# Kernel tuning notes

Measured on AMD Instinct MI355X. Metric: run time of the kernel, lower is better.

Reference implementation:

```python
import jax, jax.numpy as jnp
import numpy as np

N_AGENT = 25
N_S = 32
N_A = 4
HID = 128
EHH_HID = HID * N_AGENT          # 3200
INTER = 150                      # INTERMEDIATE_NODES
BATCH = 2048
N_EDGE = 300


def _leaky(x):
    return jnp.where(x >= 0, x, 0.01 * x)


def setup_inputs() -> dict:
    key = jax.random.key(0)
    ks = jax.random.split(key, 12)
    states = jax.random.normal(ks[0], (N_AGENT, BATCH, N_S), dtype=jnp.float32)
    ehh_w = jax.random.normal(ks[1], (N_AGENT * N_S, EHH_HID), dtype=jnp.float32) * 0.05
    anova = jax.random.normal(ks[2], (EHH_HID + INTER, N_AGENT), dtype=jnp.float32)
    w1 = jax.random.normal(ks[3], (N_AGENT, EHH_HID, 12), dtype=jnp.float32) * 0.02
    b1 = jax.random.normal(ks[4], (N_AGENT, 12), dtype=jnp.float32) * 0.02
    w2 = jax.random.normal(ks[5], (N_AGENT, 12, 12), dtype=jnp.float32) * 0.3
    b2 = jax.random.normal(ks[6], (N_AGENT, 12), dtype=jnp.float32) * 0.02
    w3 = jax.random.normal(ks[7], (N_AGENT, 12, N_A), dtype=jnp.float32) * 0.3
    b3 = jax.random.normal(ks[8], (N_AGENT, N_A), dtype=jnp.float32) * 0.02
    actions = jax.random.randint(ks[9], (N_AGENT, BATCH), 0, N_A, dtype=jnp.int32)
    # adjacency rows: (bi_att_row, neighbor_row_a, unused, neighbor_row_b)
    c0 = jax.random.randint(ks[10], (N_EDGE, 1), 0, INTER, dtype=jnp.int32)
    c13 = jax.random.randint(ks[11], (N_EDGE, 2), 0, EHH_HID, dtype=jnp.int32)
    adj = jnp.concatenate([c0, c13[:, :1], jnp.zeros((N_EDGE, 1), jnp.int32), c13[:, 1:]], axis=1)
    return {"states": states, "ehh_w": ehh_w, "anova": anova,
            "w1": w1, "b1": b1, "w2": w2, "b2": b2, "w3": w3, "b3": b3,
            "actions": actions, "adj": adj}


def reference(states, ehh_w, anova, w1, b1, w2, b2, w3, b3, actions, adj):
    # states: (A, B, S) -> ehh_s: (B, A*S)   (torch.cat(states, dim=1))
    B = states.shape[1]
    ehh_s = jnp.transpose(states, (1, 0, 2)).reshape(B, -1)
    # EHH normalization (BatchNorm, affine=False, batch stats) + linear + LeakyReLU
    mu = jnp.mean(ehh_s, axis=0, keepdims=True)
    var = jnp.var(ehh_s, axis=0, keepdims=True)
    ehh_n = (ehh_s - mu) * jax.lax.rsqrt(var + 1e-5)
    ehh_embedding = _leaky(ehh_n @ ehh_w)                    # (B, EHH_HID)

    # ANOVA attention assembly via adjacency scatter
    self_att = anova[:EHH_HID, :]                            # (EHH_HID, A)
    bi_att = anova[EHH_HID:, :]                              # (INTER, A)
    vals = bi_att[adj[:, 0], :]                              # (E, A)
    neighbor_att = jnp.zeros((EHH_HID, N_AGENT), jnp.float32)
    neighbor_att = neighbor_att.at[adj[:, 1]].set(vals)
    neighbor_att = neighbor_att.at[adj[:, 3]].set(vals)
    all_att = (self_att + neighbor_att).T                    # (A, EHH_HID)

    # att_s repeat/permute/reshape == broadcast of embedding per agent
    att_out = ehh_embedding[:, None, :] * all_att[None, :, :]  # (B, A, EHH_HID)

    # per-agent critics (ehh_hidden -> 12 -> 12 -> n_a)
    h1 = _leaky(jnp.einsum('bah,ahk->bak', att_out, w1) + b1[None])
    h2 = _leaky(jnp.einsum('bak,akj->baj', h1, w2) + b2[None])
    all_q = jnp.einsum('baj,ajc->bac', h2, w3) + b3[None]     # (B, A, N_A)

    # q = all_q.gather(1, in_acs) per agent -> (A, B)
    q = jnp.take_along_axis(all_q, actions.T[:, :, None], axis=2)[..., 0].T
    return q
```

## Files before the change

### kernel.cpp

```cpp
#include <hip/hip_runtime.h>
#include <cstdint>

#define NAG 25
#define NS 32
#define EHH 3200
#define KDIM 800
#define BATCH 2048
#define NEDGE 300
#define NPAD 384
#define KSPLIT 5

typedef _Float16 half8 __attribute__((ext_vector_type(8)));
typedef float f32x4 __attribute__((ext_vector_type(4)));

__device__ __forceinline__ float leaky(float x) { return x >= 0.f ? x : 0.01f * x; }

__global__ void init_kernel(float* __restrict__ acc, int* __restrict__ winner) {
    int t = blockIdx.x * 256 + threadIdx.x;
    if (t < 1600) acc[t] = 0.f;
    if (t < EHH) winner[t] = -1;
}

__global__ void stats_part(const float* __restrict__ states, float* __restrict__ acc) {
    int a = blockIdx.x;
    int chunk = blockIdx.y;
    int s = threadIdx.x & 31, ty = threadIdx.x >> 5;
    const float* base = states + ((size_t)a * BATCH + chunk * 128) * NS + s;
    float sum = 0.f, sq = 0.f;
    for (int b = ty; b < 128; b += 8) {
        float v = base[(size_t)b * NS];
        sum += v; sq += v * v;
    }
    __shared__ float ls[8][32], lq[8][32];
    ls[ty][s] = sum; lq[ty][s] = sq;
    __syncthreads();
    if (ty == 0) {
#pragma unroll
        for (int i = 1; i < 8; ++i) { sum += ls[i][s]; sq += lq[i][s]; }
        atomicAdd(&acc[a * 32 + s], sum);
        atomicAdd(&acc[800 + a * 32 + s], sq);
    }
}

__global__ void prep_kernel(const float* __restrict__ states, const float* __restrict__ acc,
                            const float* __restrict__ ehh_w, const int* __restrict__ adj,
                            int* __restrict__ winner,
                            _Float16* __restrict__ A, _Float16* __restrict__ wt) {
    __shared__ float tile[32][33];
    int bi = blockIdx.x;
    if (bi < 6400) {
        int t = bi * 256 + threadIdx.x;
        int b = t / KDIM;
        int f = t - b * KDIM;
        int a = f >> 5, s = f & 31;
        float m = acc[f] * (1.f / BATCH);
        float var = acc[800 + f] * (1.f / BATCH) - m * m;
        float rs = rsqrtf(var + 1e-5f);
        float v = states[((size_t)a * BATCH + b) * NS + s];
        A[t] = (_Float16)((v - m) * rs);
    } else if (bi < 8900) {
        int bb = bi - 6400;
        int n0 = (bb % 100) * 32, k0 = (bb / 100) * 32;
        int x = threadIdx.x & 31, y = threadIdx.x >> 5;
        for (int i = y; i < 32; i += 8)
            tile[i][x] = ehh_w[(size_t)(k0 + i) * EHH + n0 + x];
        __syncthreads();
        for (int i = y; i < 32; i += 8)
            wt[(size_t)(n0 + i) * KDIM + k0 + x] = (_Float16)tile[x][i];
    } else {
        int e = (bi - 8900) * 256 + threadIdx.x;
        if (e < 2 * NEDGE) {
            int pass = e >= NEDGE;
            int ee = pass ? e - NEDGE : e;
            int dest = adj[ee * 4 + (pass ? 3 : 1)];
            atomicMax(&winner[dest], e);
        }
    }
}

__global__ void w2d_kernel(const float* __restrict__ anova, const int* __restrict__ adj,
                           const int* __restrict__ winner, const float* __restrict__ w1,
                           _Float16* __restrict__ w2dt) {
    if (blockIdx.x < 313) {
        int t = blockIdx.x * 256 + threadIdx.x;
        if (t < NAG * EHH) {
            int a = t / EHH;
            int h = t - a * EHH;
            float att = anova[(size_t)h * NAG + a];
            int w = winner[h];
            if (w >= 0) {
                int ee = w >= NEDGE ? w - NEDGE : w;
                att += anova[(size_t)(EHH + adj[ee * 4]) * NAG + a];
            }
            const float* wp = w1 + ((size_t)a * EHH + h) * 12;
#pragma unroll
            for (int kk = 0; kk < 12; ++kk)
                w2dt[(size_t)(a * 12 + kk) * EHH + h] = (_Float16)(att * wp[kk]);
        }
    } else {
        int p = (blockIdx.x - 313) * 256 + threadIdx.x;
        if (p < (NPAD - 300) * EHH / 8) {
            half8 z = {0, 0, 0, 0, 0, 0, 0, 0};
            ((half8*)(w2dt + (size_t)300 * EHH))[p] = z;
        }
    }
}

__device__ __forceinline__ void async16(const void* g, void* l) {
    __builtin_amdgcn_global_load_lds(
        (const __attribute__((address_space(1))) void*)(uintptr_t)g,
        (__attribute__((address_space(3))) void*)(unsigned)(uintptr_t)l, 16, 0, 0);
}

template <bool LEAKY_F16_OUT>
__global__ __launch_bounds__(256)
void gemm_bt(const _Float16* __restrict__ A, const _Float16* __restrict__ B,
             _Float16* __restrict__ Ch, float* __restrict__ Cf,
             int Ktot, int ldc, int kPerSplit, int slabStride) {
    __shared__ __attribute__((aligned(16))) _Float16 As[2][128 * 32];
    __shared__ __attribute__((aligned(16))) _Float16 Bs[2][128 * 32];
    const int tid = threadIdx.x;
    const int lane = tid & 63;
    const int wave = tid >> 6;
    const int wm = (wave >> 1) << 6;
    const int wn = (wave & 1) << 6;
    const int m0 = blockIdx.x << 7;
    const int n0 = blockIdx.y << 7;
    const int k0 = blockIdx.z * kPerSplit;
    const int nk = kPerSplit >> 5;

    const int srow = lane >> 2;
    const int scol = (lane & 3) << 3;
    const _Float16* gA0 = A + (size_t)(m0 + wave * 16 + srow) * Ktot + k0 + scol;
    const _Float16* gA1 = gA0 + (size_t)64 * Ktot;
    const _Float16* gB0 = B + (size_t)(n0 + wave * 16 + srow) * Ktot + k0 + scol;
    const _Float16* gB1 = gB0 + (size_t)64 * Ktot;
    const int lofs = wave * 512;

    f32x4 acc[4][4];
    const f32x4 zero = {0.f, 0.f, 0.f, 0.f};
#pragma unroll
    for (int i = 0; i < 4; ++i)
#pragma unroll
        for (int j = 0; j < 4; ++j) acc[i][j] = zero;

    const int fr = lane & 15;
    const int q8 = (lane >> 4) << 3;

    async16(gA0, As[0] + lofs);
    async16(gA1, As[0] + 2048 + lofs);
    async16(gB0, Bs[0] + lofs);
    async16(gB1, Bs[0] + 2048 + lofs);

    for (int kt = 0; kt < nk; ++kt) {
        const int cur = kt & 1;
        __syncthreads();
        if (kt + 1 < nk) {
            const int ko = (kt + 1) << 5;
            const int nxt = cur ^ 1;
            async16(gA0 + ko, As[nxt] + lofs);
            async16(gA1 + ko, As[nxt] + 2048 + lofs);
            async16(gB0 + ko, Bs[nxt] + lofs);
            async16(gB1 + ko, Bs[nxt] + 2048 + lofs);
        }
        half8 av[4], bv[4];
#pragma unroll
        for (int i = 0; i < 4; ++i)
            av[i] = *(const half8*)(As[cur] + (wm + i * 16 + fr) * 32 + q8);
#pragma unroll
        for (int j = 0; j < 4; ++j)
            bv[j] = *(const half8*)(Bs[cur] + (wn + j * 16 + fr) * 32 + q8);
#pragma unroll
        for (int i = 0; i < 4; ++i)
#pragma unroll
            for (int j = 0; j < 4; ++j)
                acc[i][j] = __builtin_amdgcn_mfma_f32_16x16x32_f16(av[i], bv[j], acc[i][j], 0, 0, 0);
    }

    const int r0 = (lane >> 4) << 2;
    if (LEAKY_F16_OUT) {
#pragma unroll
        for (int i = 0; i < 4; ++i)
#pragma unroll
            for (int j = 0; j < 4; ++j)
#pragma unroll
                for (int r = 0; r < 4; ++r) {
                    int row = m0 + wm + i * 16 + r0 + r;
                    int col = n0 + wn + j * 16 + fr;
                    Ch[(size_t)row * ldc + col] = (_Float16)leaky(acc[i][j][r]);
                }
    } else {
        float* C = Cf + (size_t)blockIdx.z * slabStride;
#pragma unroll
        for (int i = 0; i < 4; ++i)
#pragma unroll
            for (int j = 0; j < 4; ++j)
#pragma unroll
                for (int r = 0; r < 4; ++r) {
                    int row = m0 + wm + i * 16 + r0 + r;
                    int col = n0 + wn + j * 16 + fr;
                    C[(size_t)row * ldc + col] = acc[i][j][r];
                }
    }
}

__global__ void tail_kernel(const float* __restrict__ Hp, const float* __restrict__ b1,
                            const float* __restrict__ w2, const float* __restrict__ b2,
                            const float* __restrict__ w3, const float* __restrict__ b3,
                            const int* __restrict__ act, float* __restrict__ out) {
    int t = blockIdx.x * 256 + threadIdx.x;
    int b = t & (BATCH - 1);
    int a = t >> 11;
    const float* hp = Hp + (size_t)b * NPAD + a * 12;
    float h1[12];
#pragma unroll
    for (int k = 0; k < 12; ++k) {
        float s = b1[a * 12 + k];
#pragma unroll
        for (int ks = 0; ks < KSPLIT; ++ks) s += hp[(size_t)ks * BATCH * NPAD + k];
        h1[k] = leaky(s);
    }
    float h2[12];
#pragma unroll
    for (int j = 0; j < 12; ++j) {
        float s = b2[a * 12 + j];
#pragma unroll
        for (int k = 0; k < 12; ++k) s += h1[k] * w2[(a * 12 + k) * 12 + j];
        h2[j] = leaky(s);
    }
    int c = act[t];
    float q = b3[a * 4 + c];
#pragma unroll
    for (int j = 0; j < 12; ++j) q += h2[j] * w3[(a * 12 + j) * 4 + c];
    out[t] = q;
}

extern "C" void kernel_launch(void* const* d_in, const int* in_sizes, int n_in,
                              void* d_out, int out_size, void* d_ws, size_t ws_size,
                              hipStream_t stream) {
    (void)in_sizes; (void)n_in; (void)out_size; (void)ws_size;
    const float* states = (const float*)d_in[0];
    const float* ehh_w  = (const float*)d_in[1];
    const float* anova  = (const float*)d_in[2];
    const float* w1     = (const float*)d_in[3];
    const float* b1     = (const float*)d_in[4];
    const float* w2     = (const float*)d_in[5];
    const float* b2     = (const float*)d_in[6];
    const float* w3     = (const float*)d_in[7];
    const float* b3     = (const float*)d_in[8];
    const int* actions  = (const int*)d_in[9];
    const int* adj      = (const int*)d_in[10];
    float* out = (float*)d_out;

    char* ws = (char*)d_ws;
    float*     acc    = (float*)    (ws + 0);
    int*       winner = (int*)      (ws + 8192);
    _Float16*  Abf    = (_Float16*) (ws + 32768);
    _Float16*  WbT    = (_Float16*) (ws + 3311616);
    _Float16*  W2dT   = (_Float16*) (ws + 8433664);
    _Float16*  emb    = (_Float16*) (ws + 10893312);
    float*     Hp     = (float*)    (ws + 24002560);

    init_kernel<<<13, 256, 0, stream>>>(acc, winner);
    stats_part<<<dim3(25, 16), 256, 0, stream>>>(states, acc);
    prep_kernel<<<8903, 256, 0, stream>>>(states, acc, ehh_w, adj, winner, Abf, WbT);
    w2d_kernel<<<445, 256, 0, stream>>>(anova, adj, winner, w1, W2dT);
    gemm_bt<true><<<dim3(16, 25, 1), 256, 0, stream>>>(Abf, WbT, emb, nullptr, KDIM, EHH, KDIM, 0);
    gemm_bt<false><<<dim3(16, 3, KSPLIT), 256, 0, stream>>>(emb, W2dT, nullptr, Hp, EHH, NPAD,
                                                            EHH / KSPLIT, BATCH * NPAD);
    tail_kernel<<<(BATCH * NAG) / 256, 256, 0, stream>>>(Hp, b1, w2, b2, w3, b3, actions, out);
}
```

Before: 143.9 us.

## Fuse all stages into one persistent kernel with software grid barriers

Replaces seven kernel launches with one persistent 256-block kernel plus a counter-init kernel, separating stages with atomic-counter grid barriers. Stats accumulation now writes per-chunk partials instead of using atomics, and the adjacency winner scan becomes a serial per-column loop. This removes launch overhead and inter-kernel gaps. In exchange the grid is limited to 256 blocks, so the large prep and GEMM stages run in a grid-stride loop with less parallelism, barrier spinning adds cost, and correctness depends on all 256 blocks being co-resident.

```diff
diff --git a/kernel.cpp b/kernel.cpp
--- a/kernel.cpp
+++ b/kernel.cpp
@@ -2,109 +2,18 @@
 #include <cstdint>
 
 #define NAG 25
-#define NS 32
 #define EHH 3200
 #define KDIM 800
 #define BATCH 2048
 #define NEDGE 300
 #define NPAD 384
 #define KSPLIT 5
+#define GRID 256
 
 typedef _Float16 half8 __attribute__((ext_vector_type(8)));
 typedef float f32x4 __attribute__((ext_vector_type(4)));
 
 __device__ __forceinline__ float leaky(float x) { return x >= 0.f ? x : 0.01f * x; }
-
-__global__ void init_kernel(float* __restrict__ acc, int* __restrict__ winner) {
-    int t = blockIdx.x * 256 + threadIdx.x;
-    if (t < 1600) acc[t] = 0.f;
-    if (t < EHH) winner[t] = -1;
-}
-
-__global__ void stats_part(const float* __restrict__ states, float* __restrict__ acc) {
-    int a = blockIdx.x;
-    int chunk = blockIdx.y;
-    int s = threadIdx.x & 31, ty = threadIdx.x >> 5;
-    const float* base = states + ((size_t)a * BATCH + chunk * 128) * NS + s;
-    float sum = 0.f, sq = 0.f;
-    for (int b = ty; b < 128; b += 8) {
-        float v = base[(size_t)b * NS];
-        sum += v; sq += v * v;
-    }
-    __shared__ float ls[8][32], lq[8][32];
-    ls[ty][s] = sum; lq[ty][s] = sq;
-    __syncthreads();
-    if (ty == 0) {
-#pragma unroll
-        for (int i = 1; i < 8; ++i) { sum += ls[i][s]; sq += lq[i][s]; }
-        atomicAdd(&acc[a * 32 + s], sum);
-        atomicAdd(&acc[800 + a * 32 + s], sq);
-    }
-}
-
-__global__ void prep_kernel(const float* __restrict__ states, const float* __restrict__ acc,
-                            const float* __restrict__ ehh_w, const int* __restrict__ adj,
-                            int* __restrict__ winner,
-                            _Float16* __restrict__ A, _Float16* __restrict__ wt) {
-    __shared__ float tile[32][33];
-    int bi = blockIdx.x;
-    if (bi < 6400) {
-        int t = bi * 256 + threadIdx.x;
-        int b = t / KDIM;
-        int f = t - b * KDIM;
-        int a = f >> 5, s = f & 31;
-        float m = acc[f] * (1.f / BATCH);
-        float var = acc[800 + f] * (1.f / BATCH) - m * m;
-        float rs = rsqrtf(var + 1e-5f);
-        float v = states[((size_t)a * BATCH + b) * NS + s];
-        A[t] = (_Float16)((v - m) * rs);
-    } else if (bi < 8900) {
-        int bb = bi - 6400;
-        int n0 = (bb % 100) * 32, k0 = (bb / 100) * 32;
-        int x = threadIdx.x & 31, y = threadIdx.x >> 5;
-        for (int i = y; i < 32; i += 8)
-            tile[i][x] = ehh_w[(size_t)(k0 + i) * EHH + n0 + x];
-        __syncthreads();
-        for (int i = y; i < 32; i += 8)
-            wt[(size_t)(n0 + i) * KDIM + k0 + x] = (_Float16)tile[x][i];
-    } else {
-        int e = (bi - 8900) * 256 + threadIdx.x;
-        if (e < 2 * NEDGE) {
-            int pass = e >= NEDGE;
-            int ee = pass ? e - NEDGE : e;
-            int dest = adj[ee * 4 + (pass ? 3 : 1)];
-            atomicMax(&winner[dest], e);
-        }
-    }
-}
-
-__global__ void w2d_kernel(const float* __restrict__ anova, const int* __restrict__ adj,
-                           const int* __restrict__ winner, const float* __restrict__ w1,
-                           _Float16* __restrict__ w2dt) {
-    if (blockIdx.x < 313) {
-        int t = blockIdx.x * 256 + threadIdx.x;
-        if (t < NAG * EHH) {
-            int a = t / EHH;
-            int h = t - a * EHH;
-            float att = anova[(size_t)h * NAG + a];
-            int w = winner[h];
-            if (w >= 0) {
-                int ee = w >= NEDGE ? w - NEDGE : w;
-                att += anova[(size_t)(EHH + adj[ee * 4]) * NAG + a];
-            }
-            const float* wp = w1 + ((size_t)a * EHH + h) * 12;
-#pragma unroll
-            for (int kk = 0; kk < 12; ++kk)
-                w2dt[(size_t)(a * 12 + kk) * EHH + h] = (_Float16)(att * wp[kk]);
-        }
-    } else {
-        int p = (blockIdx.x - 313) * 256 + threadIdx.x;
-        if (p < (NPAD - 300) * EHH / 8) {
-            half8 z = {0, 0, 0, 0, 0, 0, 0, 0};
-            ((half8*)(w2dt + (size_t)300 * EHH))[p] = z;
-        }
-    }
-}
 
 __device__ __forceinline__ void async16(const void* g, void* l) {
     __builtin_amdgcn_global_load_lds(
@@ -112,23 +21,29 @@
         (__attribute__((address_space(3))) void*)(unsigned)(uintptr_t)l, 16, 0, 0);
 }
 
+__device__ __forceinline__ void gbar(int* c) {
+    __syncthreads();
+    __threadfence();
+    if (threadIdx.x == 0) {
+        atomicAdd(c, 1);
+        while (__hip_atomic_load(c, __ATOMIC_ACQUIRE, __HIP_MEMORY_SCOPE_AGENT) < GRID)
+            __builtin_amdgcn_s_sleep(8);
+    }
+    __syncthreads();
+    __threadfence();
+}
+
+__global__ void binit(int* cnt) { if (threadIdx.x < 8) cnt[threadIdx.x] = 0; }
+
 template <bool LEAKY_F16_OUT>
-__global__ __launch_bounds__(256)
-void gemm_bt(const _Float16* __restrict__ A, const _Float16* __restrict__ B,
-             _Float16* __restrict__ Ch, float* __restrict__ Cf,
-             int Ktot, int ldc, int kPerSplit, int slabStride) {
-    __shared__ __attribute__((aligned(16))) _Float16 As[2][128 * 32];
-    __shared__ __attribute__((aligned(16))) _Float16 Bs[2][128 * 32];
-    const int tid = threadIdx.x;
+__device__ void gemm_tile(const _Float16* __restrict__ A, const _Float16* __restrict__ B,
+                          _Float16* __restrict__ Ch, float* __restrict__ Cf,
+                          int Ktot, int ldc, int nk, int m0, int n0, int k0,
+                          _Float16* As, _Float16* Bs, int tid) {
     const int lane = tid & 63;
     const int wave = tid >> 6;
     const int wm = (wave >> 1) << 6;
     const int wn = (wave & 1) << 6;
-    const int m0 = blockIdx.x << 7;
-    const int n0 = blockIdx.y << 7;
-    const int k0 = blockIdx.z * kPerSplit;
-    const int nk = kPerSplit >> 5;
-
     const int srow = lane >> 2;
     const int scol = (lane & 3) << 3;
     const _Float16* gA0 = A + (size_t)(m0 + wave * 16 + srow) * Ktot + k0 + scol;
@@ -147,29 +62,30 @@
     const int fr = lane & 15;
     const int q8 = (lane >> 4) << 3;
 
-    async16(gA0, As[0] + lofs);
-    async16(gA1, As[0] + 2048 + lofs);
-    async16(gB0, Bs[0] + lofs);
-    async16(gB1, Bs[0] + 2048 + lofs);
+    __syncthreads();
+    async16(gA0, As + lofs);
+    async16(gA1, As + 2048 + lofs);
+    async16(gB0, Bs + lofs);
+    async16(gB1, Bs + 2048 + lofs);
 
     for (int kt = 0; kt < nk; ++kt) {
-        const int cur = kt & 1;
+        const int cur = (kt & 1) * 4096;
         __syncthreads();
         if (kt + 1 < nk) {
             const int ko = (kt + 1) << 5;
-            const int nxt = cur ^ 1;
-            async16(gA0 + ko, As[nxt] + lofs);
-            async16(gA1 + ko, As[nxt] + 2048 + lofs);
-            async16(gB0 + ko, Bs[nxt] + lofs);
-            async16(gB1 + ko, Bs[nxt] + 2048 + lofs);
+            const int nxt = 4096 - cur;
+            async16(gA0 + ko, As + nxt + lofs);
+            async16(gA1 + ko, As + nxt + 2048 + lofs);
+            async16(gB0 + ko, Bs + nxt + lofs);
+            async16(gB1 + ko, Bs + nxt + 2048 + lofs);
         }
         half8 av[4], bv[4];
 #pragma unroll
         for (int i = 0; i < 4; ++i)
-            av[i] = *(const half8*)(As[cur] + (wm + i * 16 + fr) * 32 + q8);
+            av[i] = *(const half8*)(As + cur + (wm + i * 16 + fr) * 32 + q8);
 #pragma unroll
         for (int j = 0; j < 4; ++j)
-            bv[j] = *(const half8*)(Bs[cur] + (wn + j * 16 + fr) * 32 + q8);
+            bv[j] = *(const half8*)(Bs + cur + (wn + j * 16 + fr) * 32 + q8);
 #pragma unroll
         for (int i = 0; i < 4; ++i)
 #pragma unroll
@@ -178,61 +94,174 @@
     }
 
     const int r0 = (lane >> 4) << 2;
-    if (LEAKY_F16_OUT) {
-#pragma unroll
-        for (int i = 0; i < 4; ++i)
-#pragma unroll
-            for (int j = 0; j < 4; ++j)
-#pragma unroll
-                for (int r = 0; r < 4; ++r) {
-                    int row = m0 + wm + i * 16 + r0 + r;
-                    int col = n0 + wn + j * 16 + fr;
+#pragma unroll
+    for (int i = 0; i < 4; ++i)
+#pragma unroll
+        for (int j = 0; j < 4; ++j)
+#pragma unroll
+            for (int r = 0; r < 4; ++r) {
+                int row = m0 + wm + i * 16 + r0 + r;
+                int col = n0 + wn + j * 16 + fr;
+                if (LEAKY_F16_OUT)
                     Ch[(size_t)row * ldc + col] = (_Float16)leaky(acc[i][j][r]);
-                }
-    } else {
-        float* C = Cf + (size_t)blockIdx.z * slabStride;
-#pragma unroll
-        for (int i = 0; i < 4; ++i)
-#pragma unroll
-            for (int j = 0; j < 4; ++j)
-#pragma unroll
-                for (int r = 0; r < 4; ++r) {
-                    int row = m0 + wm + i * 16 + r0 + r;
-                    int col = n0 + wn + j * 16 + fr;
-                    C[(size_t)row * ldc + col] = acc[i][j][r];
-                }
-    }
-}
-
-__global__ void tail_kernel(const float* __restrict__ Hp, const float* __restrict__ b1,
-                            const float* __restrict__ w2, const float* __restrict__ b2,
-                            const float* __restrict__ w3, const float* __restrict__ b3,
-                            const int* __restrict__ act, float* __restrict__ out) {
-    int t = blockIdx.x * 256 + threadIdx.x;
-    int b = t & (BATCH - 1);
-    int a = t >> 11;
-    const float* hp = Hp + (size_t)b * NPAD + a * 12;
-    float h1[12];
-#pragma unroll
-    for (int k = 0; k < 12; ++k) {
-        float s = b1[a * 12 + k];
-#pragma unroll
-        for (int ks = 0; ks < KSPLIT; ++ks) s += hp[(size_t)ks * BATCH * NPAD + k];
-        h1[k] = leaky(s);
-    }
-    float h2[12];
-#pragma unroll
-    for (int j = 0; j < 12; ++j) {
-        float s = b2[a * 12 + j];
-#pragma unroll
-        for (int k = 0; k < 12; ++k) s += h1[k] * w2[(a * 12 + k) * 12 + j];
-        h2[j] = leaky(s);
-    }
-    int c = act[t];
-    float q = b3[a * 4 + c];
-#pragma unroll
-    for (int j = 0; j < 12; ++j) q += h2[j] * w3[(a * 12 + j) * 4 + c];
-    out[t] = q;
+                else
+                    Cf[(size_t)row * ldc + col] = acc[i][j][r];
+            }
+}
+
+__global__ __launch_bounds__(256, 2)
+void mega(const float* __restrict__ states, const float* __restrict__ ehh_w,
+          const float* __restrict__ anova, const float* __restrict__ w1,
+          const float* __restrict__ b1, const float* __restrict__ w2,
+          const float* __restrict__ b2, const float* __restrict__ w3,
+          const float* __restrict__ b3, const int* __restrict__ actions,
+          const int* __restrict__ adj, float* __restrict__ out,
+          char* __restrict__ ws) {
+    __shared__ __attribute__((aligned(16))) char smem[32768];
+    float*     pacc = (float*)ws;
+    float*     mrs  = (float*)(ws + 102400);
+    int*       wsrc = (int*)(ws + 108800);
+    int*       cnt  = (int*)(ws + 121600);
+    _Float16*  Abf  = (_Float16*)(ws + 122880);
+    _Float16*  WbT  = (_Float16*)(ws + 3399680);
+    _Float16*  W2dT = (_Float16*)(ws + 8519680);
+    _Float16*  emb  = (_Float16*)(ws + 10977280);
+    float*     Hp   = (float*)(ws + 24084480);
+
+    const int tid = threadIdx.x;
+    const int bid = blockIdx.x;
+
+    for (int vt = bid; vt < 400; vt += GRID) {
+        float* ls = (float*)smem;
+        float* lq = ls + 256;
+        int a = vt % 25, chunk = vt / 25;
+        int s = tid & 31, ty = tid >> 5;
+        const float* base = states + ((size_t)a * BATCH + chunk * 128) * 32 + s;
+        float sum = 0.f, sq = 0.f;
+        for (int b = ty; b < 128; b += 8) {
+            float v = base[(size_t)b * 32];
+            sum += v; sq += v * v;
+        }
+        __syncthreads();
+        ls[ty * 32 + s] = sum; lq[ty * 32 + s] = sq;
+        __syncthreads();
+        if (ty == 0) {
+#pragma unroll
+            for (int i = 1; i < 8; ++i) { sum += ls[i * 32 + s]; sq += lq[i * 32 + s]; }
+            pacc[chunk * 800 + a * 32 + s] = sum;
+            pacc[12800 + chunk * 800 + a * 32 + s] = sq;
+        }
+    }
+    gbar(cnt + 0);
+
+    if (bid < 4) {
+        int f = bid * 256 + tid;
+        if (f < 800) {
+            float s = 0.f, q = 0.f;
+#pragma unroll
+            for (int c = 0; c < 16; ++c) { s += pacc[c * 800 + f]; q += pacc[12800 + c * 800 + f]; }
+            float m = s * (1.f / BATCH);
+            float var = q * (1.f / BATCH) - m * m;
+            mrs[f] = m;
+            mrs[800 + f] = rsqrtf(var + 1e-5f);
+        }
+    } else if (bid < 17) {
+        int h = (bid - 4) * 256 + tid;
+        if (h < EHH) {
+            int win = -1;
+            for (int e = 0; e < NEDGE; ++e) if (adj[e * 4 + 1] == h) win = e;
+            for (int e = 0; e < NEDGE; ++e) if (adj[e * 4 + 3] == h) win = NEDGE + e;
+            wsrc[h] = win >= 0 ? adj[(win >= NEDGE ? win - NEDGE : win) * 4] : -1;
+        }
+    }
+    gbar(cnt + 1);
+
+    for (int vt = bid; vt < 9345; vt += GRID) {
+        if (vt < 6400) {
+            int t = vt * 256 + tid;
+            int b = t / KDIM;
+            int f = t - b * KDIM;
+            int a = f >> 5, s = f & 31;
+            float v = states[((size_t)a * BATCH + b) * 32 + s];
+            Abf[t] = (_Float16)((v - mrs[f]) * mrs[800 + f]);
+        } else if (vt < 8900) {
+            float* tile = (float*)smem;
+            int bb = vt - 6400;
+            int n0 = (bb % 100) * 32, k0 = (bb / 100) * 32;
+            int x = tid & 31, y = tid >> 5;
+            __syncthreads();
+            for (int i = y; i < 32; i += 8)
+                tile[i * 33 + x] = ehh_w[(size_t)(k0 + i) * EHH + n0 + x];
+            __syncthreads();
+            for (int i = y; i < 32; i += 8)
+                WbT[(size_t)(n0 + i) * KDIM + k0 + x] = (_Float16)tile[x * 33 + i];
+        } else if (vt < 9213) {
+            int t = (vt - 8900) * 256 + tid;
+            if (t < NAG * EHH) {
+                int a = t / EHH, h = t - a * EHH;
+                float att = anova[(size_t)h * NAG + a];
+                int src = wsrc[h];
+                if (src >= 0) att += anova[(size_t)(EHH + src) * NAG + a];
+                const float* wp = w1 + ((size_t)a * EHH + h) * 12;
+#pragma unroll
+                for (int kk = 0; kk < 12; ++kk)
+                    W2dT[(size_t)(a * 12 + kk) * EHH + h] = (_Float16)(att * wp[kk]);
+            }
+        } else {
+            int p = (vt - 9213) * 256 + tid;
+            if (p < (NPAD - 300) * EHH / 8) {
+                half8 z = {0, 0, 0, 0, 0, 0, 0, 0};
+                ((half8*)(W2dT + (size_t)300 * EHH))[p] = z;
+            }
+        }
+    }
+    gbar(cnt + 2);
+
+    _Float16* As = (_Float16*)smem;
+    _Float16* Bs = As + 8192;
+    for (int vt = bid; vt < 400; vt += GRID) {
+        int m0 = (vt & 15) << 7;
+        int n0 = (vt >> 4) << 7;
+        gemm_tile<true>(Abf, WbT, emb, nullptr, KDIM, EHH, 25, m0, n0, 0, As, Bs, tid);
+    }
+    gbar(cnt + 3);
+
+    if (bid < 240) {
+        int m0 = (bid & 15) << 7;
+        int n0 = ((bid >> 4) % 3) << 7;
+        int bz = bid / 48;
+        gemm_tile<false>(emb, W2dT, nullptr, Hp + (size_t)bz * BATCH * NPAD,
+                         EHH, NPAD, EHH / KSPLIT / 32, m0, n0, bz * (EHH / KSPLIT), As, Bs, tid);
+    }
+    gbar(cnt + 4);
+
+    if (bid < 200) {
+        int t = bid * 256 + tid;
+        int b = t & (BATCH - 1);
+        int a = t >> 11;
+        const float* hp = Hp + (size_t)b * NPAD + a * 12;
+        float h1v[12];
+#pragma unroll
+        for (int k = 0; k < 12; ++k) {
+            float s = b1[a * 12 + k];
+#pragma unroll
+            for (int ks = 0; ks < KSPLIT; ++ks) s += hp[(size_t)ks * BATCH * NPAD + k];
+            h1v[k] = leaky(s);
+        }
+        float h2v[12];
+#pragma unroll
+        for (int j = 0; j < 12; ++j) {
+            float s = b2[a * 12 + j];
+#pragma unroll
+            for (int k = 0; k < 12; ++k) s += h1v[k] * w2[(a * 12 + k) * 12 + j];
+            h2v[j] = leaky(s);
+        }
+        int c = actions[t];
+        float q = b3[a * 4 + c];
+#pragma unroll
+        for (int j = 0; j < 12; ++j) q += h2v[j] * w3[(a * 12 + j) * 4 + c];
+        out[t] = q;
+    }
 }
 
 extern "C" void kernel_launch(void* const* d_in, const int* in_sizes, int n_in,
@@ -251,22 +280,10 @@
     const int* actions  = (const int*)d_in[9];
     const int* adj      = (const int*)d_in[10];
     float* out = (float*)d_out;
-
     char* ws = (char*)d_ws;
-    float*     acc    = (float*)    (ws + 0);
-    int*       winner = (int*)      (ws + 8192);
-    _Float16*  Abf    = (_Float16*) (ws + 32768);
-    _Float16*  WbT    = (_Float16*) (ws + 3311616);
-    _Float16*  W2dT   = (_Float16*) (ws + 8433664);
-    _Float16*  emb    = (_Float16*) (ws + 10893312);
-    float*     Hp     = (float*)    (ws + 24002560);
-
-    init_kernel<<<13, 256, 0, stream>>>(acc, winner);
-    stats_part<<<dim3(25, 16), 256, 0, stream>>>(states, acc);
-    prep_kernel<<<8903, 256, 0, stream>>>(states, acc, ehh_w, adj, winner, Abf, WbT);
-    w2d_kernel<<<445, 256, 0, stream>>>(anova, adj, winner, w1, W2dT);
-    gemm_bt<true><<<dim3(16, 25, 1), 256, 0, stream>>>(Abf, WbT, emb, nullptr, KDIM, EHH, KDIM, 0);
-    gemm_bt<false><<<dim3(16, 3, KSPLIT), 256, 0, stream>>>(emb, W2dT, nullptr, Hp, EHH, NPAD,
-                                                            EHH / KSPLIT, BATCH * NPAD);
-    tail_kernel<<<(BATCH * NAG) / 256, 256, 0, stream>>>(Hp, b1, w2, b2, w3, b3, actions, out);
-}
+    int* cnt = (int*)(ws + 121600);
+
+    binit<<<1, 256, 0, stream>>>(cnt);
+    mega<<<GRID, 256, 0, stream>>>(states, ehh_w, anova, w1, b1, w2, b2, w3, b3,
+                                   actions, adj, out, ws);
+}
```

New measurement: 536.4 us. 3.73x slower.

## Fuse prep and attention-weight kernels, replace atomics with partial sums

Applied to the files above, without the earlier changes.

The init and w2d kernels are removed: batch statistics become per-chunk partial sums that prep_kernel reduces itself, and the attention-folded W1 build moves into prep_kernel. The edge 'winner' per hidden unit is found by a per-thread linear scan of the adjacency, replacing the atomicMax pass. This cuts two launches, the zero-init pass and the atomics. In exchange each thread does 600 serial uniform adjacency reads. The tail kernel's thread mapping also changes so Hp reads are contiguous, at the cost of strided output and action accesses.

```diff
diff --git a/kernel.cpp b/kernel.cpp
--- a/kernel.cpp
+++ b/kernel.cpp
@@ -2,7 +2,6 @@
 #include <cstdint>
 
 #define NAG 25
-#define NS 32
 #define EHH 3200
 #define KDIM 800
 #define BATCH 2048
@@ -15,20 +14,14 @@
 
 __device__ __forceinline__ float leaky(float x) { return x >= 0.f ? x : 0.01f * x; }
 
-__global__ void init_kernel(float* __restrict__ acc, int* __restrict__ winner) {
-    int t = blockIdx.x * 256 + threadIdx.x;
-    if (t < 1600) acc[t] = 0.f;
-    if (t < EHH) winner[t] = -1;
-}
-
-__global__ void stats_part(const float* __restrict__ states, float* __restrict__ acc) {
+__global__ void stats_part(const float* __restrict__ states, float* __restrict__ pacc) {
     int a = blockIdx.x;
     int chunk = blockIdx.y;
     int s = threadIdx.x & 31, ty = threadIdx.x >> 5;
-    const float* base = states + ((size_t)a * BATCH + chunk * 128) * NS + s;
+    const float* base = states + ((size_t)a * BATCH + chunk * 128) * 32 + s;
     float sum = 0.f, sq = 0.f;
     for (int b = ty; b < 128; b += 8) {
-        float v = base[(size_t)b * NS];
+        float v = base[(size_t)b * 32];
         sum += v; sq += v * v;
     }
     __shared__ float ls[8][32], lq[8][32];
@@ -37,68 +30,58 @@
     if (ty == 0) {
 #pragma unroll
         for (int i = 1; i < 8; ++i) { sum += ls[i][s]; sq += lq[i][s]; }
-        atomicAdd(&acc[a * 32 + s], sum);
-        atomicAdd(&acc[800 + a * 32 + s], sq);
-    }
-}
-
-__global__ void prep_kernel(const float* __restrict__ states, const float* __restrict__ acc,
-                            const float* __restrict__ ehh_w, const int* __restrict__ adj,
-                            int* __restrict__ winner,
-                            _Float16* __restrict__ A, _Float16* __restrict__ wt) {
+        pacc[chunk * 800 + a * 32 + s] = sum;
+        pacc[12800 + chunk * 800 + a * 32 + s] = sq;
+    }
+}
+
+__global__ void prep_kernel(const float* __restrict__ states, const float* __restrict__ pacc,
+                            const float* __restrict__ ehh_w, const float* __restrict__ anova,
+                            const int* __restrict__ adj, const float* __restrict__ w1,
+                            _Float16* __restrict__ A, _Float16* __restrict__ wt,
+                            _Float16* __restrict__ w2dt) {
     __shared__ float tile[32][33];
-    int bi = blockIdx.x;
-    if (bi < 6400) {
-        int t = bi * 256 + threadIdx.x;
+    int vt = blockIdx.x;
+    int tid = threadIdx.x;
+    if (vt < 6400) {
+        int t = vt * 256 + tid;
         int b = t / KDIM;
         int f = t - b * KDIM;
         int a = f >> 5, s = f & 31;
-        float m = acc[f] * (1.f / BATCH);
-        float var = acc[800 + f] * (1.f / BATCH) - m * m;
+        float su = 0.f, sq = 0.f;
+#pragma unroll
+        for (int c = 0; c < 16; ++c) { su += pacc[c * 800 + f]; sq += pacc[12800 + c * 800 + f]; }
+        float m = su * (1.f / BATCH);
+        float var = sq * (1.f / BATCH) - m * m;
         float rs = rsqrtf(var + 1e-5f);
-        float v = states[((size_t)a * BATCH + b) * NS + s];
+        float v = states[((size_t)a * BATCH + b) * 32 + s];
         A[t] = (_Float16)((v - m) * rs);
-    } else if (bi < 8900) {
-        int bb = bi - 6400;
+    } else if (vt < 8900) {
+        int bb = vt - 6400;
         int n0 = (bb % 100) * 32, k0 = (bb / 100) * 32;
-        int x = threadIdx.x & 31, y = threadIdx.x >> 5;
+        int x = tid & 31, y = tid >> 5;
         for (int i = y; i < 32; i += 8)
             tile[i][x] = ehh_w[(size_t)(k0 + i) * EHH + n0 + x];
         __syncthreads();
         for (int i = y; i < 32; i += 8)
             wt[(size_t)(n0 + i) * KDIM + k0 + x] = (_Float16)tile[x][i];
-    } else {
-        int e = (bi - 8900) * 256 + threadIdx.x;
-        if (e < 2 * NEDGE) {
-            int pass = e >= NEDGE;
-            int ee = pass ? e - NEDGE : e;
-            int dest = adj[ee * 4 + (pass ? 3 : 1)];
-            atomicMax(&winner[dest], e);
-        }
-    }
-}
-
-__global__ void w2d_kernel(const float* __restrict__ anova, const int* __restrict__ adj,
-                           const int* __restrict__ winner, const float* __restrict__ w1,
-                           _Float16* __restrict__ w2dt) {
-    if (blockIdx.x < 313) {
-        int t = blockIdx.x * 256 + threadIdx.x;
+    } else if (vt < 9213) {
+        int t = (vt - 8900) * 256 + tid;
         if (t < NAG * EHH) {
-            int a = t / EHH;
-            int h = t - a * EHH;
+            int a = t / EHH, h = t - a * EHH;
+            int win = -1;
+            for (int e = 0; e < NEDGE; ++e) if (adj[e * 4 + 1] == h) win = e;
+            for (int e = 0; e < NEDGE; ++e) if (adj[e * 4 + 3] == h) win = NEDGE + e;
             float att = anova[(size_t)h * NAG + a];
-            int w = winner[h];
-            if (w >= 0) {
-                int ee = w >= NEDGE ? w - NEDGE : w;
-                att += anova[(size_t)(EHH + adj[ee * 4]) * NAG + a];
-            }
+            if (win >= 0)
+                att += anova[(size_t)(EHH + adj[(win >= NEDGE ? win - NEDGE : win) * 4]) * NAG + a];
             const float* wp = w1 + ((size_t)a * EHH + h) * 12;
 #pragma unroll
             for (int kk = 0; kk < 12; ++kk)
                 w2dt[(size_t)(a * 12 + kk) * EHH + h] = (_Float16)(att * wp[kk]);
         }
     } else {
-        int p = (blockIdx.x - 313) * 256 + threadIdx.x;
+        int p = (vt - 9213) * 256 + tid;
         if (p < (NPAD - 300) * EHH / 8) {
             half8 z = {0, 0, 0, 0, 0, 0, 0, 0};
             ((half8*)(w2dt + (size_t)300 * EHH))[p] = z;
@@ -178,30 +161,19 @@
     }
 
     const int r0 = (lane >> 4) << 2;
-    if (LEAKY_F16_OUT) {
-#pragma unroll
-        for (int i = 0; i < 4; ++i)
-#pragma unroll
-            for (int j = 0; j < 4; ++j)
-#pragma unroll
-                for (int r = 0; r < 4; ++r) {
-                    int row = m0 + wm + i * 16 + r0 + r;
-                    int col = n0 + wn + j * 16 + fr;
+#pragma unroll
+    for (int i = 0; i < 4; ++i)
+#pragma unroll
+        for (int j = 0; j < 4; ++j)
+#pragma unroll
+            for (int r = 0; r < 4; ++r) {
+                int row = m0 + wm + i * 16 + r0 + r;
+                int col = n0 + wn + j * 16 + fr;
+                if (LEAKY_F16_OUT)
                     Ch[(size_t)row * ldc + col] = (_Float16)leaky(acc[i][j][r]);
-                }
-    } else {
-        float* C = Cf + (size_t)blockIdx.z * slabStride;
-#pragma unroll
-        for (int i = 0; i < 4; ++i)
-#pragma unroll
-            for (int j = 0; j < 4; ++j)
-#pragma unroll
-                for (int r = 0; r < 4; ++r) {
-                    int row = m0 + wm + i * 16 + r0 + r;
-                    int col = n0 + wn + j * 16 + fr;
-                    C[(size_t)row * ldc + col] = acc[i][j][r];
-                }
-    }
+                else
+                    Cf[(size_t)blockIdx.z * slabStride + (size_t)row * ldc + col] = acc[i][j][r];
+            }
 }
 
 __global__ void tail_kernel(const float* __restrict__ Hp, const float* __restrict__ b1,
@@ -209,8 +181,8 @@
                             const float* __restrict__ w3, const float* __restrict__ b3,
                             const int* __restrict__ act, float* __restrict__ out) {
     int t = blockIdx.x * 256 + threadIdx.x;
-    int b = t & (BATCH - 1);
-    int a = t >> 11;
+    int b = t / NAG;
+    int a = t - b * NAG;
     const float* hp = Hp + (size_t)b * NPAD + a * 12;
     float h1[12];
 #pragma unroll
@@ -228,11 +200,11 @@
         for (int k = 0; k < 12; ++k) s += h1[k] * w2[(a * 12 + k) * 12 + j];
         h2[j] = leaky(s);
     }
-    int c = act[t];
+    int c = act[a * BATCH + b];
     float q = b3[a * 4 + c];
 #pragma unroll
     for (int j = 0; j < 12; ++j) q += h2[j] * w3[(a * 12 + j) * 4 + c];
-    out[t] = q;
+    out[a * BATCH + b] = q;
 }
 
 extern "C" void kernel_launch(void* const* d_in, const int* in_sizes, int n_in,
@@ -253,18 +225,15 @@
     float* out = (float*)d_out;
 
     char* ws = (char*)d_ws;
-    float*     acc    = (float*)    (ws + 0);
-    int*       winner = (int*)      (ws + 8192);
-    _Float16*  Abf    = (_Float16*) (ws + 32768);
-    _Float16*  WbT    = (_Float16*) (ws + 3311616);
-    _Float16*  W2dT   = (_Float16*) (ws + 8433664);
-    _Float16*  emb    = (_Float16*) (ws + 10893312);
-    float*     Hp     = (float*)    (ws + 24002560);
-
-    init_kernel<<<13, 256, 0, stream>>>(acc, winner);
-    stats_part<<<dim3(25, 16), 256, 0, stream>>>(states, acc);
-    prep_kernel<<<8903, 256, 0, stream>>>(states, acc, ehh_w, adj, winner, Abf, WbT);
-    w2d_kernel<<<445, 256, 0, stream>>>(anova, adj, winner, w1, W2dT);
+    float*     pacc = (float*)    (ws + 0);
+    _Float16*  Abf  = (_Float16*) (ws + 102400);
+    _Float16*  WbT  = (_Float16*) (ws + 3379200);
+    _Float16*  W2dT = (_Float16*) (ws + 8499200);
+    _Float16*  emb  = (_Float16*) (ws + 10956800);
+    float*     Hp   = (float*)    (ws + 24064000);
+
+    stats_part<<<dim3(25, 16), 256, 0, stream>>>(states, pacc);
+    prep_kernel<<<9345, 256, 0, stream>>>(states, pacc, ehh_w, anova, adj, w1, Abf, WbT, W2dT);
     gemm_bt<true><<<dim3(16, 25, 1), 256, 0, stream>>>(Abf, WbT, emb, nullptr, KDIM, EHH, KDIM, 0);
     gemm_bt<false><<<dim3(16, 3, KSPLIT), 256, 0, stream>>>(emb, W2dT, nullptr, Hp, EHH, NPAD,
                                                             EHH / KSPLIT, BATCH * NPAD);
```

After: 178.6 us. 1.24x slower.
